# Performance work log

Hardware: AMD Instinct MI355X
Metric: run time of the kernel (lower is better)

## Reference

```python
import jax, jax.numpy as jnp
import numpy as np


def _pairwise_dist(x):
    # ||xi - xj||_2 via Gram trick: sq_ij = |xi|^2 + |xj|^2 - 2 xi.xj  (exact same math,
    # avoids the O(n^2*d) broadcast intermediate of the torch code)
    sq_norms = jnp.sum(x * x, axis=1)  # [n]
    gram = x @ x.T                      # [n, n]
    sq = jnp.maximum(sq_norms[:, None] + sq_norms[None, :] - 2.0 * gram, 0.0)
    # safe sqrt: zero distance (diagonal) stays exactly 0 with well-defined grad
    pos = sq > 0
    return jnp.where(pos, jnp.sqrt(jnp.where(pos, sq, 1.0)), 0.0)


def _double_center(a):
    # A = a - colmean - rowmean + grandmean
    return a - jnp.mean(a, axis=0)[None, :] - jnp.mean(a, axis=1)[:, None] + jnp.mean(a)


def setup_inputs() -> dict:
    key = jax.random.key(0)
    kx, ky = jax.random.split(key)
    x = jax.random.normal(kx, (8192, 128), dtype=jnp.float32)
    y = jax.random.normal(ky, (8192, 128), dtype=jnp.float32)
    return {"x": x, "y": y}


def reference(x, y):
    n = x.shape[0]
    A = _double_center(_pairwise_dist(x))  # [n, n]
    B = _double_center(_pairwise_dist(y))  # [n, n]
    inv_n2 = 1.0 / float(n * n)
    dcov2_xy = jnp.sum(A * B) * inv_n2
    dcov2_xx = jnp.sum(A * A) * inv_n2
    dcov2_yy = jnp.sum(B * B) * inv_n2
    dcor = -jnp.sqrt(dcov2_xy) / jnp.sqrt(jnp.sqrt(dcov2_xx) * jnp.sqrt(dcov2_yy))
    return dcor
```

## Files before the change

### kernel.cpp

```cpp
#include <hip/hip_runtime.h>


typedef float f32x4 __attribute__((ext_vector_type(4)));
typedef __bf16 bf16x8 __attribute__((ext_vector_type(8)));

#define NR 8192
#define D 128
#define TILE 128
#define GB 64
#define NT 2080
#define BK 64

#define OFF_YB  2097152u
#define OFF_NX  4194304u
#define OFF_NY  (OFF_NX + 32768u)
#define OFF_RPX (OFF_NY + 32768u)
#define OFF_RPY (OFF_RPX + 2097152u)
#define OFF_PP  (OFF_RPY + 2097152u)
#define OFF_SB  (OFF_PP + 49920u)
#define WS_NEED (OFF_SB + 2560u)

#define GLOAD_LDS16(g, l)                                                  \
    __builtin_amdgcn_global_load_lds(                                      \
        (const __attribute__((address_space(1))) unsigned*)(g),            \
        (__attribute__((address_space(3))) unsigned*)(l), 16, 0, 0)

__device__ __forceinline__ unsigned short bf16_rne(float f) {
    union { float f; unsigned u; } c; c.f = f;
    unsigned u = c.u;
    u += 0x7FFFu + ((u >> 16) & 1u);
    return (unsigned short)(u >> 16);
}

__global__ __launch_bounds__(256) void prep_kernel(
    const float* __restrict__ x, const float* __restrict__ y,
    unsigned short* __restrict__ xb, unsigned short* __restrict__ yb,
    float* __restrict__ nx, float* __restrict__ ny)
{
    int gid = blockIdx.x * 256 + threadIdx.x;
    int wave = gid >> 6;
    int lane = threadIdx.x & 63;
    const float* src; unsigned short* db; float* dn; int row;
    if (wave < NR) { src = x; db = xb; dn = nx; row = wave; }
    else           { src = y; db = yb; dn = ny; row = wave - NR; }

    const float2 v = *reinterpret_cast<const float2*>(src + (size_t)row * D + lane * 2);
    float s = v.x * v.x + v.y * v.y;
    unsigned packed = (unsigned)bf16_rne(v.x) | ((unsigned)bf16_rne(v.y) << 16);
    int h = lane >> 5, q = (lane >> 2) & 7, o = (lane & 3) * 2;
    int sidx = h * 64 + ((q ^ (row & 7)) << 3) + o;
    *reinterpret_cast<unsigned*>(db + (size_t)row * D + sidx) = packed;
#pragma unroll
    for (int m = 1; m < 64; m <<= 1) s += __shfl_xor(s, m);
    if (lane == 0) dn[row] = s;
}

#define BSTEP(arr, S) {                                                    \
    const int b_ = (lrow >> (S)) & 1;                                      \
    _Pragma("unroll")                                                      \
    for (int i_ = 0; i_ < (8 >> (S)); ++i_) {                              \
        float k_ = b_ ? arr[2 * i_ + 1] : arr[2 * i_];                     \
        float s_ = b_ ? arr[2 * i_] : arr[2 * i_ + 1];                     \
        arr[i_] = k_ + __shfl_xor(s_, 1 << (S));                           \
    } }

__global__ __launch_bounds__(512) void dcor_main6(
    const unsigned short* __restrict__ xb, const unsigned short* __restrict__ yb,
    const float* __restrict__ nx, const float* __restrict__ ny,
    float* __restrict__ RPx, float* __restrict__ RPy,
    double* __restrict__ Pp )
{
    const int t = (blockIdx.x & 7) * (NT / 8) + (blockIdx.x >> 3);
    double qd = 2.0 * GB + 1.0;
    int bi = (int)((qd - sqrt(qd * qd - 8.0 * (double)t)) * 0.5);
    while (bi > 0 && bi * GB - bi * (bi - 1) / 2 > t) --bi;
    while ((bi + 1) * GB - (bi + 1) * bi / 2 <= t) ++bi;
    const int bj = bi + (t - (bi * GB - bi * (bi - 1) / 2));
    const bool diag = (bi == bj);

    __shared__ __align__(16) unsigned short Buf[2][2][TILE][BK];
    __shared__ float nl[4][TILE];
    __shared__ float rsum[4][TILE];
    __shared__ float pr[3][8];

    const int tid  = threadIdx.x;
    const int lane = tid & 63, wid = tid >> 6;
    const int wr = wid >> 2, wc = wid & 3;
    const int lrow = lane & 15, lkb = lane >> 4;

    if (tid < TILE) {
        nl[0][tid] = nx[bi * TILE + tid];
        nl[1][tid] = nx[bj * TILE + tid];
        nl[2][tid] = ny[bi * TILE + tid];
        nl[3][tid] = ny[bj * TILE + tid];
        rsum[0][tid] = 0.f; rsum[1][tid] = 0.f;
        rsum[2][tid] = 0.f; rsum[3][tid] = 0.f;
    }

    auto stage = [&](int b, const unsigned short* srcb, int h) {
        const char* gb = (const char*)srcb;
#pragma unroll
        for (int it = 0; it < 4; ++it) {
            int s = wid * 4 + it;
            int tsel = s >> 4;
            int r0 = (s & 15) * 8;
            unsigned short* ldsb = &Buf[b][tsel][r0][0];
            int grow = (tsel ? bj : bi) * TILE + r0 + (lane >> 3);
            const char* g = gb + (size_t)grow * 256 + h * 128 + (lane & 7) * 16;
            GLOAD_LDS16(g, ldsb);
        }
    };

    auto gram = [&](int b, f32x4 (&acc)[4][2]) {
        const char* Ti = (const char*)&Buf[b][0][0][0];
        const char* Tj = (const char*)&Buf[b][1][0][0];
#pragma unroll
        for (int kk = 0; kk < 2; ++kk) {
            const int sA = (((kk << 2) | lkb) ^ (lrow & 7)) << 4;
            bf16x8 a[4], bb[2];
#pragma unroll
            for (int m = 0; m < 4; ++m) {
                int row = wr * 64 + m * 16 + lrow;
                a[m] = *reinterpret_cast<const bf16x8*>(Ti + row * 128 + sA);
            }
#pragma unroll
            for (int nf = 0; nf < 2; ++nf) {
                int row = wc * 32 + nf * 16 + lrow;
                bb[nf] = *reinterpret_cast<const bf16x8*>(Tj + row * 128 + sA);
            }
#pragma unroll
            for (int m = 0; m < 4; ++m)
#pragma unroll
                for (int nf = 0; nf < 2; ++nf)
                    acc[m][nf] = __builtin_amdgcn_mfma_f32_16x16x32_bf16(
                        a[m], bb[nf], acc[m][nf], 0, 0, 0);
        }
    };

    auto to_dist = [&](f32x4 (&acc)[4][2], const float* nRw, const float* nC) {
        const float nc0 = nC[wc * 32 + lrow];
        const float nc1 = nC[wc * 32 + 16 + lrow];
#pragma unroll
        for (int m = 0; m < 4; ++m) {
            float nr[4];
#pragma unroll
            for (int r = 0; r < 4; ++r)
                nr[r] = nRw[wr * 64 + m * 16 + lkb * 4 + r];
#pragma unroll
            for (int nf = 0; nf < 2; ++nf) {
                const float nc = nf ? nc1 : nc0;
#pragma unroll
                for (int r = 0; r < 4; ++r) {
                    float sq = nr[r] + nc - 2.f * acc[m][nf][r];
                    acc[m][nf][r] = __builtin_amdgcn_sqrtf(fmaxf(sq, 0.f));
                }
            }
        }
        if (diag) {
#pragma unroll
            for (int m = 0; m < 4; ++m)
#pragma unroll
                for (int nf = 0; nf < 2; ++nf)
#pragma unroll
                    for (int r = 0; r < 4; ++r) {
                        int row_l = wr * 64 + m * 16 + lkb * 4 + r;
                        int col_l = wc * 32 + nf * 16 + lrow;
                        if (row_l == col_l) acc[m][nf][r] = 0.f;
                    }
        }
    };

    const f32x4 fz = {0.f, 0.f, 0.f, 0.f};
    f32x4 accX[4][2], accY[4][2];
#pragma unroll
    for (int m = 0; m < 4; ++m)
#pragma unroll
        for (int nf = 0; nf < 2; ++nf) { accX[m][nf] = fz; accY[m][nf] = fz; }

    stage(0, xb, 0);
    __syncthreads();
    stage(1, xb, 1);
    gram(0, accX);
    __syncthreads();
    stage(0, yb, 0);
    gram(1, accX);
    to_dist(accX, nl[0], nl[1]);
    __syncthreads();
    stage(1, yb, 1);
    gram(0, accY);
    __syncthreads();
    gram(1, accY);
    to_dist(accY, nl[2], nl[3]);

    float pxy = 0.f, pxx = 0.f, pyy = 0.f;
    float ax[16], ay[16];
    float csx[2] = {0.f, 0.f}, csy[2] = {0.f, 0.f};
#pragma unroll
    for (int j = 0; j < 16; ++j) { ax[j] = 0.f; ay[j] = 0.f; }

#pragma unroll
    for (int m = 0; m < 4; ++m)
#pragma unroll
        for (int nf = 0; nf < 2; ++nf)
#pragma unroll
            for (int r = 0; r < 4; ++r) {
                float dx = accX[m][nf][r], dy = accY[m][nf][r];
                pxy += dx * dy;
                pxx += dx * dx;
                pyy += dy * dy;
                ax[m * 4 + r] += dx;  ay[m * 4 + r] += dy;
                csx[nf] += dx;        csy[nf] += dy;
            }

    BSTEP(ax, 0) BSTEP(ay, 0)
    BSTEP(ax, 1) BSTEP(ay, 1)
    BSTEP(ax, 2) BSTEP(ay, 2)
    BSTEP(ax, 3) BSTEP(ay, 3)
    {
        int row_l = wr * 64 + ((lrow >> 2) << 4) + (lkb << 2) + (lrow & 3);
        atomicAdd(&rsum[0][row_l], ax[0]);
        atomicAdd(&rsum[1][row_l], ay[0]);
    }
#pragma unroll
    for (int nf = 0; nf < 2; ++nf) {
        float vx = csx[nf], vy = csy[nf];
        vx += __shfl_xor(vx, 16); vx += __shfl_xor(vx, 32);
        vy += __shfl_xor(vy, 16); vy += __shfl_xor(vy, 32);
        if (lkb == 0) {
            int col_l = wc * 32 + nf * 16 + lrow;
            atomicAdd(&rsum[2][col_l], vx);
            atomicAdd(&rsum[3][col_l], vy);
        }
    }
#pragma unroll
    for (int m = 1; m < 64; m <<= 1) {
        pxy += __shfl_xor(pxy, m);
        pxx += __shfl_xor(pxx, m);
        pyy += __shfl_xor(pyy, m);
    }
    if (lane == 0) { pr[0][wid] = pxy; pr[1][wid] = pxx; pr[2][wid] = pyy; }
    __syncthreads();

    if (tid == 0) {
        double sxy = 0, sxx = 0, syy = 0;
#pragma unroll
        for (int w = 0; w < 8; ++w) {
            sxy += (double)pr[0][w]; sxx += (double)pr[1][w]; syy += (double)pr[2][w];
        }
        double sc = diag ? 1.0 : 2.0;
        Pp[t] = sxy * sc;
        Pp[NT + t] = sxx * sc;
        Pp[2 * NT + t] = syy * sc;
    }
    if (tid < TILE) {
        RPx[((size_t)bi * GB + bj) * TILE + tid] = rsum[0][tid];
        RPy[((size_t)bi * GB + bj) * TILE + tid] = rsum[1][tid];
        if (!diag) {
            RPx[((size_t)bj * GB + bi) * TILE + tid] = rsum[2][tid];
            RPy[((size_t)bj * GB + bi) * TILE + tid] = rsum[3][tid];
        }
    }
}

__global__ __launch_bounds__(128) void row_reduce2(
    const float* __restrict__ RPx, const float* __restrict__ RPy,
    double* __restrict__ SB )
{
    int b = blockIdx.x, t = threadIdx.x;
    double rx = 0.0, ry = 0.0;
    for (int k = 0; k < GB; ++k) {
        rx += (double)RPx[((size_t)b * GB + k) * TILE + t];
        ry += (double)RPy[((size_t)b * GB + k) * TILE + t];
    }
    double s0 = rx, s1 = ry, s2 = rx * ry, s3 = rx * rx, s4 = ry * ry;
#pragma unroll
    for (int m = 1; m < 64; m <<= 1) {
        s0 += __shfl_xor(s0, m); s1 += __shfl_xor(s1, m);
        s2 += __shfl_xor(s2, m); s3 += __shfl_xor(s3, m);
        s4 += __shfl_xor(s4, m);
    }
    __shared__ double sb[5][2];
    int lane = t & 63, w = t >> 6;
    if (lane == 0) { sb[0][w] = s0; sb[1][w] = s1; sb[2][w] = s2; sb[3][w] = s3; sb[4][w] = s4; }
    __syncthreads();
    if (t == 0)
#pragma unroll
        for (int i = 0; i < 5; ++i) SB[b * 5 + i] = sb[i][0] + sb[i][1];
}

__global__ __launch_bounds__(256) void dcor_final3(
    const double* __restrict__ SB, const double* __restrict__ Pp,
    unsigned* __restrict__ out)
{
    double sx = 0, sy = 0, sxy = 0, sxx = 0, syy = 0, pxy = 0, pxx = 0, pyy = 0;
    for (int b = threadIdx.x; b < GB; b += 256) {
        sx += SB[b * 5]; sy += SB[b * 5 + 1]; sxy += SB[b * 5 + 2];
        sxx += SB[b * 5 + 3]; syy += SB[b * 5 + 4];
    }
    for (int b = threadIdx.x; b < NT; b += 256) {
        pxy += Pp[b]; pxx += Pp[NT + b]; pyy += Pp[2 * NT + b];
    }
    __shared__ double red[8][4];
    int lane = threadIdx.x & 63, w = threadIdx.x >> 6;
#pragma unroll
    for (int m = 1; m < 64; m <<= 1) {
        sx += __shfl_xor(sx, m);  sy += __shfl_xor(sy, m);
        sxy += __shfl_xor(sxy, m); sxx += __shfl_xor(sxx, m); syy += __shfl_xor(syy, m);
        pxy += __shfl_xor(pxy, m); pxx += __shfl_xor(pxx, m); pyy += __shfl_xor(pyy, m);
    }
    if (lane == 0) {
        red[0][w] = sx;  red[1][w] = sy;  red[2][w] = sxy; red[3][w] = sxx;
        red[4][w] = syy; red[5][w] = pxy; red[6][w] = pxx; red[7][w] = pyy;
    }
    __syncthreads();
    if (threadIdx.x == 0) {
        sx  = red[0][0] + red[0][1] + red[0][2] + red[0][3];
        sy  = red[1][0] + red[1][1] + red[1][2] + red[1][3];
        sxy = red[2][0] + red[2][1] + red[2][2] + red[2][3];
        sxx = red[3][0] + red[3][1] + red[3][2] + red[3][3];
        syy = red[4][0] + red[4][1] + red[4][2] + red[4][3];
        pxy = red[5][0] + red[5][1] + red[5][2] + red[5][3];
        pxx = red[6][0] + red[6][1] + red[6][2] + red[6][3];
        pyy = red[7][0] + red[7][1] + red[7][2] + red[7][3];
        const double inv = 1.0 / (double)NR;
        double vxy = pxy - 2.0 * inv * sxy + sx * sy * inv * inv;
        double vxx = pxx - 2.0 * inv * sxx + sx * sx * inv * inv;
        double vyy = pyy - 2.0 * inv * syy + sy * sy * inv * inv;
        vxy = fmax(vxy, 0.0);
        vxx = fmax(vxx, 1e-30); vyy = fmax(vyy, 1e-30);
        double dcor = -sqrt(vxy) / sqrt(sqrt(vxx) * sqrt(vyy));
        unsigned short b = bf16_rne((float)dcor);
        out[0] = ((unsigned)b << 16) | (unsigned)b;
    }
}

extern "C" void kernel_launch(void* const* d_in, const int* in_sizes, int n_in,
                              void* d_out, int out_size, void* d_ws, size_t ws_size,
                              hipStream_t stream)
{
    const float* x = (const float*)d_in[0];
    const float* y = (const float*)d_in[1];
    char* ws = (char*)d_ws;
    unsigned short* xb = (unsigned short*)(ws);
    unsigned short* yb = (unsigned short*)(ws + OFF_YB);
    float* nx = (float*)(ws + OFF_NX);
    float* ny = (float*)(ws + OFF_NY);
    float* RPx = (float*)(ws + OFF_RPX);
    float* RPy = (float*)(ws + OFF_RPY);
    double* Pp = (double*)(ws + OFF_PP);
    double* SB = (double*)(ws + OFF_SB);

    prep_kernel<<<4096, 256, 0, stream>>>(x, y, xb, yb, nx, ny);
    dcor_main6<<<NT, 512, 0, stream>>>(xb, yb, nx, ny, RPx, RPy, Pp);
    row_reduce2<<<GB, 128, 0, stream>>>(RPx, RPy, SB);
    dcor_final3<<<1, 256, 0, stream>>>(SB, Pp, (unsigned*)d_out);
}
```

Measured before the change: 97.65 us.

## Load MFMA operands directly from global memory instead of LDS staging

Removes the LDS double-buffer and its global_load_lds staging with barriers. Each wave now reads bf16x8 fragments for the gram MFMAs straight from global memory, relying on L1/L2 for reuse. The swizzle in the prep kernel is dropped because the layout is now plain row-major. This cuts LDS traffic and synchronisation, but each tile is re-read from global/cache by several waves, and the 256-byte row stride gives uncoalesced per-lane 16-byte loads.

```diff
diff --git a/kernel.cpp b/kernel.cpp
--- a/kernel.cpp
+++ b/kernel.cpp
@@ -9,7 +9,6 @@
 #define TILE 128
 #define GB 64
 #define NT 2080
-#define BK 64
 
 #define OFF_YB  2097152u
 #define OFF_NX  4194304u
@@ -20,11 +19,6 @@
 #define OFF_SB  (OFF_PP + 49920u)
 #define WS_NEED (OFF_SB + 2560u)
 
-#define GLOAD_LDS16(g, l)                                                  \
-    __builtin_amdgcn_global_load_lds(                                      \
-        (const __attribute__((address_space(1))) unsigned*)(g),            \
-        (__attribute__((address_space(3))) unsigned*)(l), 16, 0, 0)
-
 __device__ __forceinline__ unsigned short bf16_rne(float f) {
     union { float f; unsigned u; } c; c.f = f;
     unsigned u = c.u;
@@ -47,9 +41,7 @@
     const float2 v = *reinterpret_cast<const float2*>(src + (size_t)row * D + lane * 2);
     float s = v.x * v.x + v.y * v.y;
     unsigned packed = (unsigned)bf16_rne(v.x) | ((unsigned)bf16_rne(v.y) << 16);
-    int h = lane >> 5, q = (lane >> 2) & 7, o = (lane & 3) * 2;
-    int sidx = h * 64 + ((q ^ (row & 7)) << 3) + o;
-    *reinterpret_cast<unsigned*>(db + (size_t)row * D + sidx) = packed;
+    *reinterpret_cast<unsigned*>(db + (size_t)row * D + lane * 2) = packed;
 #pragma unroll
     for (int m = 1; m < 64; m <<= 1) s += __shfl_xor(s, m);
     if (lane == 0) dn[row] = s;
@@ -64,7 +56,7 @@
         arr[i_] = k_ + __shfl_xor(s_, 1 << (S));                           \
     } }
 
-__global__ __launch_bounds__(512) void dcor_main6(
+__global__ __launch_bounds__(512) void dcor_main7(
     const unsigned short* __restrict__ xb, const unsigned short* __restrict__ yb,
     const float* __restrict__ nx, const float* __restrict__ ny,
     float* __restrict__ RPx, float* __restrict__ RPy,
@@ -78,7 +70,6 @@
     const int bj = bi + (t - (bi * GB - bi * (bi - 1) / 2));
     const bool diag = (bi == bj);
 
-    __shared__ __align__(16) unsigned short Buf[2][2][TILE][BK];
     __shared__ float nl[4][TILE];
     __shared__ float rsum[4][TILE];
     __shared__ float pr[3][8];
@@ -96,44 +87,33 @@
         rsum[0][tid] = 0.f; rsum[1][tid] = 0.f;
         rsum[2][tid] = 0.f; rsum[3][tid] = 0.f;
     }
-
-    auto stage = [&](int b, const unsigned short* srcb, int h) {
-        const char* gb = (const char*)srcb;
-#pragma unroll
-        for (int it = 0; it < 4; ++it) {
-            int s = wid * 4 + it;
-            int tsel = s >> 4;
-            int r0 = (s & 15) * 8;
-            unsigned short* ldsb = &Buf[b][tsel][r0][0];
-            int grow = (tsel ? bj : bi) * TILE + r0 + (lane >> 3);
-            const char* g = gb + (size_t)grow * 256 + h * 128 + (lane & 7) * 16;
-            GLOAD_LDS16(g, ldsb);
-        }
-    };
-
-    auto gram = [&](int b, f32x4 (&acc)[4][2]) {
-        const char* Ti = (const char*)&Buf[b][0][0][0];
-        const char* Tj = (const char*)&Buf[b][1][0][0];
-#pragma unroll
-        for (int kk = 0; kk < 2; ++kk) {
-            const int sA = (((kk << 2) | lkb) ^ (lrow & 7)) << 4;
-            bf16x8 a[4], bb[2];
-#pragma unroll
-            for (int m = 0; m < 4; ++m) {
-                int row = wr * 64 + m * 16 + lrow;
-                a[m] = *reinterpret_cast<const bf16x8*>(Ti + row * 128 + sA);
-            }
-#pragma unroll
-            for (int nf = 0; nf < 2; ++nf) {
-                int row = wc * 32 + nf * 16 + lrow;
-                bb[nf] = *reinterpret_cast<const bf16x8*>(Tj + row * 128 + sA);
-            }
+    __syncthreads();
+
+    int aoff[4], boff[2];
+#pragma unroll
+    for (int m = 0; m < 4; ++m)
+        aoff[m] = (wr * 64 + m * 16 + lrow) * 256 + lkb * 16;
+#pragma unroll
+    for (int nf = 0; nf < 2; ++nf)
+        boff[nf] = (wc * 32 + nf * 16 + lrow) * 256 + lkb * 16;
+
+    auto gram = [&](const char* TiB, const char* TjB, f32x4 (&acc)[4][2]) {
+#pragma unroll
+        for (int kk = 0; kk < 4; ++kk) {
+            const int ko = kk * 64;
+            bf16x8 a[4], b[2];
+#pragma unroll
+            for (int m = 0; m < 4; ++m)
+                a[m] = *reinterpret_cast<const bf16x8*>(TiB + aoff[m] + ko);
+#pragma unroll
+            for (int nf = 0; nf < 2; ++nf)
+                b[nf] = *reinterpret_cast<const bf16x8*>(TjB + boff[nf] + ko);
 #pragma unroll
             for (int m = 0; m < 4; ++m)
 #pragma unroll
                 for (int nf = 0; nf < 2; ++nf)
                     acc[m][nf] = __builtin_amdgcn_mfma_f32_16x16x32_bf16(
-                        a[m], bb[nf], acc[m][nf], 0, 0, 0);
+                        a[m], b[nf], acc[m][nf], 0, 0, 0);
         }
     };
 
@@ -177,19 +157,14 @@
 #pragma unroll
         for (int nf = 0; nf < 2; ++nf) { accX[m][nf] = fz; accY[m][nf] = fz; }
 
-    stage(0, xb, 0);
-    __syncthreads();
-    stage(1, xb, 1);
-    gram(0, accX);
-    __syncthreads();
-    stage(0, yb, 0);
-    gram(1, accX);
+    const char* TiX = (const char*)xb + (size_t)bi * TILE * 256;
+    const char* TjX = (const char*)xb + (size_t)bj * TILE * 256;
+    const char* TiY = (const char*)yb + (size_t)bi * TILE * 256;
+    const char* TjY = (const char*)yb + (size_t)bj * TILE * 256;
+
+    gram(TiX, TjX, accX);
     to_dist(accX, nl[0], nl[1]);
-    __syncthreads();
-    stage(1, yb, 1);
-    gram(0, accY);
-    __syncthreads();
-    gram(1, accY);
+    gram(TiY, TjY, accY);
     to_dist(accY, nl[2], nl[3]);
 
     float pxy = 0.f, pxx = 0.f, pyy = 0.f;
@@ -351,7 +326,7 @@
     double* SB = (double*)(ws + OFF_SB);
 
     prep_kernel<<<4096, 256, 0, stream>>>(x, y, xb, yb, nx, ny);
-    dcor_main6<<<NT, 512, 0, stream>>>(xb, yb, nx, ny, RPx, RPy, Pp);
+    dcor_main7<<<NT, 512, 0, stream>>>(xb, yb, nx, ny, RPx, RPy, Pp);
     row_reduce2<<<GB, 128, 0, stream>>>(RPx, RPy, SB);
     dcor_final3<<<1, 256, 0, stream>>>(SB, Pp, (unsigned*)d_out);
 }
```

Result: slower. 149.2 us (+52.8%).

## Shrink LDS K-chunk to 32 and double pipeline stages for gram tiles

Applied to the files above, without the earlier changes.

Each staging step now loads a 32-wide K slice of both the i and j tiles into one interleaved 128x64 buffer, with the XOR swizzle applied at load time instead of in the prep kernel's global layout. This cuts shared memory per block by half, which may allow more resident blocks per CU to hide latency, and precomputes the per-lane LDS byte offsets. The cost is twice as many stage/sync steps, with one MFMA k-step per barrier instead of two, so synchronisation overhead rises.

```diff
diff --git a/kernel.cpp b/kernel.cpp
--- a/kernel.cpp
+++ b/kernel.cpp
@@ -9,7 +9,6 @@
 #define TILE 128
 #define GB 64
 #define NT 2080
-#define BK 64
 
 #define OFF_YB  2097152u
 #define OFF_NX  4194304u
@@ -47,9 +46,7 @@
     const float2 v = *reinterpret_cast<const float2*>(src + (size_t)row * D + lane * 2);
     float s = v.x * v.x + v.y * v.y;
     unsigned packed = (unsigned)bf16_rne(v.x) | ((unsigned)bf16_rne(v.y) << 16);
-    int h = lane >> 5, q = (lane >> 2) & 7, o = (lane & 3) * 2;
-    int sidx = h * 64 + ((q ^ (row & 7)) << 3) + o;
-    *reinterpret_cast<unsigned*>(db + (size_t)row * D + sidx) = packed;
+    *reinterpret_cast<unsigned*>(db + (size_t)row * D + lane * 2) = packed;
 #pragma unroll
     for (int m = 1; m < 64; m <<= 1) s += __shfl_xor(s, m);
     if (lane == 0) dn[row] = s;
@@ -64,7 +61,7 @@
         arr[i_] = k_ + __shfl_xor(s_, 1 << (S));                           \
     } }
 
-__global__ __launch_bounds__(512) void dcor_main6(
+__global__ __launch_bounds__(512) void dcor_main8(
     const unsigned short* __restrict__ xb, const unsigned short* __restrict__ yb,
     const float* __restrict__ nx, const float* __restrict__ ny,
     float* __restrict__ RPx, float* __restrict__ RPy,
@@ -78,7 +75,7 @@
     const int bj = bi + (t - (bi * GB - bi * (bi - 1) / 2));
     const bool diag = (bi == bj);
 
-    __shared__ __align__(16) unsigned short Buf[2][2][TILE][BK];
+    __shared__ __align__(16) unsigned short Buf[2][TILE][64];
     __shared__ float nl[4][TILE];
     __shared__ float rsum[4][TILE];
     __shared__ float pr[3][8];
@@ -97,44 +94,46 @@
         rsum[2][tid] = 0.f; rsum[3][tid] = 0.f;
     }
 
-    auto stage = [&](int b, const unsigned short* srcb, int h) {
+    auto stage = [&](int b, const unsigned short* srcb, int kc) {
         const char* gb = (const char*)srcb;
 #pragma unroll
-        for (int it = 0; it < 4; ++it) {
-            int s = wid * 4 + it;
-            int tsel = s >> 4;
-            int r0 = (s & 15) * 8;
-            unsigned short* ldsb = &Buf[b][tsel][r0][0];
-            int grow = (tsel ? bj : bi) * TILE + r0 + (lane >> 3);
-            const char* g = gb + (size_t)grow * 256 + h * 128 + (lane & 7) * 16;
-            GLOAD_LDS16(g, ldsb);
+        for (int it = 0; it < 2; ++it) {
+            int s = wid * 2 + it;
+            int row = s * 8 + (lane >> 3);
+            int c = (lane & 7) ^ (row & 7);
+            int pr_ = (c < 4 ? bi : bj) * TILE + row;
+            const char* g = gb + (size_t)pr_ * 256 + kc * 64 + (c & 3) * 16;
+            GLOAD_LDS16(g, &Buf[b][s * 8][0]);
         }
     };
 
+    int abyte[4], bbyte[2];
+#pragma unroll
+    for (int m = 0; m < 4; ++m) {
+        int r = wr * 64 + m * 16 + lrow;
+        abyte[m] = r * 128 + (lkb ^ (r & 7)) * 16;
+    }
+#pragma unroll
+    for (int nf = 0; nf < 2; ++nf) {
+        int r = wc * 32 + nf * 16 + lrow;
+        bbyte[nf] = r * 128 + ((4 | lkb) ^ (r & 7)) * 16;
+    }
+
     auto gram = [&](int b, f32x4 (&acc)[4][2]) {
-        const char* Ti = (const char*)&Buf[b][0][0][0];
-        const char* Tj = (const char*)&Buf[b][1][0][0];
-#pragma unroll
-        for (int kk = 0; kk < 2; ++kk) {
-            const int sA = (((kk << 2) | lkb) ^ (lrow & 7)) << 4;
-            bf16x8 a[4], bb[2];
-#pragma unroll
-            for (int m = 0; m < 4; ++m) {
-                int row = wr * 64 + m * 16 + lrow;
-                a[m] = *reinterpret_cast<const bf16x8*>(Ti + row * 128 + sA);
-            }
-#pragma unroll
-            for (int nf = 0; nf < 2; ++nf) {
-                int row = wc * 32 + nf * 16 + lrow;
-                bb[nf] = *reinterpret_cast<const bf16x8*>(Tj + row * 128 + sA);
-            }
-#pragma unroll
-            for (int m = 0; m < 4; ++m)
-#pragma unroll
-                for (int nf = 0; nf < 2; ++nf)
-                    acc[m][nf] = __builtin_amdgcn_mfma_f32_16x16x32_bf16(
-                        a[m], bb[nf], acc[m][nf], 0, 0, 0);
-        }
+        const char* base = (const char*)&Buf[b][0][0];
+        bf16x8 a[4], bb[2];
+#pragma unroll
+        for (int m = 0; m < 4; ++m)
+            a[m] = *reinterpret_cast<const bf16x8*>(base + abyte[m]);
+#pragma unroll
+        for (int nf = 0; nf < 2; ++nf)
+            bb[nf] = *reinterpret_cast<const bf16x8*>(base + bbyte[nf]);
+#pragma unroll
+        for (int m = 0; m < 4; ++m)
+#pragma unroll
+            for (int nf = 0; nf < 2; ++nf)
+                acc[m][nf] = __builtin_amdgcn_mfma_f32_16x16x32_bf16(
+                    a[m], bb[nf], acc[m][nf], 0, 0, 0);
     };
 
     auto to_dist = [&](f32x4 (&acc)[4][2], const float* nRw, const float* nC) {
@@ -179,15 +178,20 @@
 
     stage(0, xb, 0);
     __syncthreads();
-    stage(1, xb, 1);
-    gram(0, accX);
-    __syncthreads();
-    stage(0, yb, 0);
-    gram(1, accX);
+    stage(1, xb, 1); gram(0, accX);
+    __syncthreads();
+    stage(0, xb, 2); gram(1, accX);
+    __syncthreads();
+    stage(1, xb, 3); gram(0, accX);
+    __syncthreads();
+    stage(0, yb, 0); gram(1, accX);
     to_dist(accX, nl[0], nl[1]);
     __syncthreads();
-    stage(1, yb, 1);
-    gram(0, accY);
+    stage(1, yb, 1); gram(0, accY);
+    __syncthreads();
+    stage(0, yb, 2); gram(1, accY);
+    __syncthreads();
+    stage(1, yb, 3); gram(0, accY);
     __syncthreads();
     gram(1, accY);
     to_dist(accY, nl[2], nl[3]);
@@ -351,7 +355,7 @@
     double* SB = (double*)(ws + OFF_SB);
 
     prep_kernel<<<4096, 256, 0, stream>>>(x, y, xb, yb, nx, ny);
-    dcor_main6<<<NT, 512, 0, stream>>>(xb, yb, nx, ny, RPx, RPy, Pp);
+    dcor_main8<<<NT, 512, 0, stream>>>(xb, yb, nx, ny, RPx, RPy, Pp);
     row_reduce2<<<GB, 128, 0, stream>>>(RPx, RPy, SB);
     dcor_final3<<<1, 256, 0, stream>>>(SB, Pp, (unsigned*)d_out);
 }
```

Result: slower. 100.1 us (+2.5%).
